# Performance work log

Hardware: AMD Instinct MI355X
Metric: run time of the kernel (lower is better)

## Reference

```python
import jax, jax.numpy as jnp
import numpy as np

NUM_HEADS = 16
SOFTPLUS_EPS = 1e-4


def rotate_half(x):
    x1, x2 = jnp.split(x, 2, axis=-1)
    return jnp.concatenate((-x2, x1), axis=-1)


def setup_inputs() -> dict:
    key = jax.random.key(0)
    B, S, H = 1, 2048, 2048
    D = H // NUM_HEADS  # 128
    ks = jax.random.split(key, 5)
    hidden_states = jax.random.normal(ks[0], (B, S, H), dtype=jnp.float32)
    # standard RoPE tables: [S, D]
    inv_freq = 1.0 / (10000.0 ** (np.arange(0, D, 2, dtype=np.float32) / D))
    freqs = np.outer(np.arange(S, dtype=np.float32), inv_freq)  # [S, D/2]
    emb = np.concatenate([freqs, freqs], axis=-1)  # [S, D]
    cos = jnp.asarray(np.cos(emb), dtype=jnp.float32)
    sin = jnp.asarray(np.sin(emb), dtype=jnp.float32)
    std = 0.02
    w_q = jax.random.normal(ks[1], (2 * H, H), dtype=jnp.float32) * std
    w_k = jax.random.normal(ks[2], (2 * H, H), dtype=jnp.float32) * std
    w_v = jax.random.normal(ks[3], (H, H), dtype=jnp.float32) * std
    w_o = jax.random.normal(ks[4], (H, H), dtype=jnp.float32) * std
    return {"hidden_states": hidden_states, "cos": cos, "sin": sin,
            "w_q": w_q, "w_k": w_k, "w_v": w_v, "w_o": w_o}


def reference(hidden_states, cos, sin, w_q, w_k, w_v, w_o):
    B, S, H = hidden_states.shape
    NH = NUM_HEADS
    D = H // NH
    # projections (torch Linear: y = x @ W.T)
    q = (hidden_states @ w_q.T).reshape(B, S, NH, 2 * D).swapaxes(1, 2)  # [B,NH,S,2D]
    k = (hidden_states @ w_k.T).reshape(B, S, NH, 2 * D).swapaxes(1, 2)
    v = (hidden_states @ w_v.T).reshape(B, S, NH, D).swapaxes(1, 2)      # [B,NH,S,D]
    q_mu, q_sigma_raw = jnp.split(q, 2, axis=-1)
    k_mu, k_sigma_raw = jnp.split(k, 2, axis=-1)
    q_sigma = jax.nn.softplus(q_sigma_raw) + SOFTPLUS_EPS
    k_sigma = jax.nn.softplus(k_sigma_raw) + SOFTPLUS_EPS
    q_w = q_mu / jnp.sqrt(q_sigma)
    k_w = k_mu / jnp.sqrt(k_sigma)
    # RoPE on variance-weighted means; cos/sin [S,D] broadcast over [B,NH,S,D]
    q_w = q_w * cos + rotate_half(q_w) * sin
    k_w = k_w * cos + rotate_half(k_w) * sin
    q_sq = jnp.sum(q_w * q_w, axis=-1, keepdims=True)          # [B,NH,S,1]
    k_sq = jnp.sum(k_w * k_w, axis=-1, keepdims=True)          # [B,NH,S,1]
    dot = jnp.einsum('bhqd,bhkd->bhqk', q_w, k_w)              # [B,NH,S,S]
    weighted_dist = q_sq + jnp.swapaxes(k_sq, -2, -1) - 2.0 * dot
    log_det_q = jnp.sum(jnp.log(q_sigma), axis=-1, keepdims=True)
    log_det_k = jnp.sum(jnp.log(k_sigma), axis=-1, keepdims=True)
    log_det = log_det_q + jnp.swapaxes(log_det_k, -2, -1)
    attn_scores = -0.5 * (weighted_dist + log_det)
    attn_probs = jax.nn.softmax(attn_scores, axis=-1)
    attn_out = jnp.einsum('bhqk,bhkd->bhqd', attn_probs, v)    # [B,NH,S,D]
    attn_out = attn_out.swapaxes(1, 2).reshape(B, S, H)
    return attn_out @ w_o.T
```

## Files before the change

### kernel.cpp

```cpp
#include <hip/hip_runtime.h>
#include <stdint.h>

#define S_LEN 2048
#define HID   2048
#define NHEAD 16
#define HD    128
#define NQK   8192
#define K_HID 2048

typedef _Float16 f16x8 __attribute__((ext_vector_type(8)));
typedef float    f32x4 __attribute__((ext_vector_type(4)));

__device__ __forceinline__ unsigned short f2h(float f) {
    _Float16 h = (_Float16)f;
    union { _Float16 h; unsigned short u; } c; c.h = h;
    return c.u;
}
__device__ __forceinline__ float h2f(unsigned short b) {
    union { unsigned short u; _Float16 h; } c; c.u = b;
    return (float)c.h;
}
__device__ __forceinline__ float softplus_f(float x) {
    return (x > 20.f) ? x : log1pf(expf(x));
}
__device__ __forceinline__ unsigned pk2h(float a, float b) {
    auto w = __builtin_amdgcn_cvt_pkrtz(a, b);
    union { decltype(w) h; unsigned u; } c; c.h = w;
    return c.u;
}
#define EXP2F(x) __builtin_amdgcn_exp2f(x)
#define LOG2E 1.44269504088896f
__device__ __forceinline__ void gload_lds16(const unsigned short* g, unsigned short* l) {
    __builtin_amdgcn_global_load_lds(
        (const __attribute__((address_space(1))) unsigned int*)g,
        (__attribute__((address_space(3))) unsigned int*)l, 16, 0, 0);
}
__device__ __forceinline__ void bar() {
    asm volatile("" ::: "memory");
    __builtin_amdgcn_s_barrier();
    asm volatile("" ::: "memory");
}
#define VMCNT(n) asm volatile("s_waitcnt vmcnt(" #n ")" ::: "memory")

__global__ __launch_bounds__(256) void cast5(const float* __restrict__ hs,
                                             const float* __restrict__ wq,
                                             const float* __restrict__ wk,
                                             const float* __restrict__ wv,
                                             const float* __restrict__ wo,
                                             unsigned short* __restrict__ hs16,
                                             unsigned short* __restrict__ wqk16,
                                             unsigned short* __restrict__ wv16,
                                             unsigned short* __restrict__ wo16) {
    int b = blockIdx.x;
    const float* src;
    unsigned short* dst;
    int i;
    if (b < 4096)       { src = hs; dst = hs16;                          i = b; }
    else if (b < 12288) { src = wq; dst = wqk16;                         i = b - 4096; }
    else if (b < 20480) { src = wk; dst = wqk16 + (size_t)4096 * K_HID;  i = b - 12288; }
    else if (b < 24576) { src = wv; dst = wv16;                          i = b - 20480; }
    else                { src = wo; dst = wo16;                          i = b - 24576; }
    int idx = i * 256 + threadIdx.x;
    float4 v = ((const float4*)src)[idx];
    ushort4 o;
    o.x = f2h(v.x); o.y = f2h(v.y); o.z = f2h(v.z); o.w = f2h(v.w);
    ((ushort4*)dst)[idx] = o;
}

template <bool OUT_F16>
__device__ __forceinline__ void gemm_body(const unsigned short* __restrict__ A,
                                          const unsigned short* __restrict__ B,
                                          void* __restrict__ Cv,
                                          int m0, int n0, int N,
                                          unsigned short* As, unsigned short* Bs) {
    const int t    = threadIdx.x;
    const int wave = t >> 6;
    const int lane = t & 63;
    const int wm   = wave >> 1, wn = wave & 1;
    const int lrow = lane & 15, quad = lane >> 4;
    const int srow = lane >> 2;
    const int scol = (lane & 3) * 8;

    f32x4 acc[4][4];
    for (int i = 0; i < 4; ++i)
        for (int j = 0; j < 4; ++j)
            acc[i][j] = (f32x4){0.f, 0.f, 0.f, 0.f};

    for (int k0 = 0; k0 < K_HID; k0 += 32) {
        for (int c = 0; c < 2; ++c) {
            int ch = wave * 2 + c;
            int row = ch * 16 + srow;
            gload_lds16(A + (size_t)(m0 + row) * K_HID + k0 + scol, &As[ch * 512]);
            gload_lds16(B + (size_t)(n0 + row) * K_HID + k0 + scol, &Bs[ch * 512]);
        }
        __syncthreads();

        f16x8 af[4], bfr[4];
        for (int tm = 0; tm < 4; ++tm)
            af[tm]  = *(const f16x8*)(&As[(wm * 64 + tm * 16 + lrow) * 32 + quad * 8]);
        for (int tn = 0; tn < 4; ++tn)
            bfr[tn] = *(const f16x8*)(&Bs[(wn * 64 + tn * 16 + lrow) * 32 + quad * 8]);
        for (int tm = 0; tm < 4; ++tm)
            for (int tn = 0; tn < 4; ++tn)
                acc[tm][tn] = __builtin_amdgcn_mfma_f32_16x16x32_f16(af[tm], bfr[tn], acc[tm][tn], 0, 0, 0);
        __syncthreads();
    }

    for (int tm = 0; tm < 4; ++tm)
        for (int tn = 0; tn < 4; ++tn) {
            int col = n0 + wn * 64 + tn * 16 + lrow;
            for (int r = 0; r < 4; ++r) {
                int row = m0 + wm * 64 + tm * 16 + quad * 4 + r;
                if (OUT_F16)
                    ((unsigned short*)Cv)[(size_t)row * N + col] = f2h(acc[tm][tn][r]);
                else
                    ((float*)Cv)[(size_t)row * N + col] = acc[tm][tn][r];
            }
        }
}

__device__ __forceinline__ void prep_body(int gid, int lane,
                                          const unsigned short* __restrict__ qk,
                                          const float* __restrict__ cosb,
                                          const float* __restrict__ sinb,
                                          unsigned short* __restrict__ Q16,
                                          unsigned short* __restrict__ K16,
                                          float* __restrict__ kbias) {
    int h = gid >> 11;
    int s = gid & 2047;
    int d1 = lane, d2 = lane + 64;
    const unsigned short* row = qk + (size_t)s * NQK;
    float c1 = cosb[s * HD + d1], c2 = cosb[s * HD + d2];
    float s1 = sinb[s * HD + d1], s2 = sinb[s * HD + d2];
    size_t ob = ((size_t)h * S_LEN + s) * HD;

    {
        int base = h * 256;
        float mu1 = h2f(row[base + d1]),       mu2 = h2f(row[base + d2]);
        float sg1 = softplus_f(h2f(row[base + 128 + d1])) + 1e-4f;
        float sg2 = softplus_f(h2f(row[base + 128 + d2])) + 1e-4f;
        float w1 = mu1 * rsqrtf(sg1), w2 = mu2 * rsqrtf(sg2);
        float o1 = w1 * c1 - w2 * s1;
        float o2 = w2 * c2 + w1 * s2;
        Q16[ob + d1] = f2h(o1 * LOG2E);
        Q16[ob + d2] = f2h(o2 * LOG2E);
    }
    {
        int base = 4096 + h * 256;
        float mu1 = h2f(row[base + d1]),       mu2 = h2f(row[base + d2]);
        float sg1 = softplus_f(h2f(row[base + 128 + d1])) + 1e-4f;
        float sg2 = softplus_f(h2f(row[base + 128 + d2])) + 1e-4f;
        float w1 = mu1 * rsqrtf(sg1), w2 = mu2 * rsqrtf(sg2);
        float o1 = w1 * c1 - w2 * s1;
        float o2 = w2 * c2 + w1 * s2;
        unsigned short k1 = f2h(o1), k2 = f2h(o2);
        K16[ob + d1] = k1; K16[ob + d2] = k2;
        float r1 = h2f(k1), r2 = h2f(k2);
        float part = r1 * r1 + r2 * r2 + logf(sg1) + logf(sg2);
        for (int off = 32; off > 0; off >>= 1) part += __shfl_down(part, off);
        if (lane == 0) kbias[(size_t)h * S_LEN + s] = -0.5f * LOG2E * part;
    }
}

__global__ __launch_bounds__(256) void gemm_qkv(const unsigned short* __restrict__ hs16,
                                                const unsigned short* __restrict__ wqk16,
                                                const unsigned short* __restrict__ wv16,
                                                unsigned short* __restrict__ qk16,
                                                unsigned short* __restrict__ Vt) {
    __shared__ __align__(16) unsigned short As[128 * 32];
    __shared__ __align__(16) unsigned short Bs[128 * 32];
    int b = blockIdx.x;
    if (b < 1024) {
        gemm_body<true>(hs16, wqk16, qk16, (b >> 6) * 128, (b & 63) * 128, NQK, As, Bs);
    } else {
        b -= 1024;
        gemm_body<true>(wv16, hs16, Vt, (b >> 4) * 128, (b & 15) * 128, S_LEN, As, Bs);
    }
}

template <bool OUT_F16>
__global__ __launch_bounds__(256) void gemm_nt_f16(const unsigned short* __restrict__ A,
                                                   const unsigned short* __restrict__ B,
                                                   void* __restrict__ Cv,
                                                   int M, int N, int Kd) {
    __shared__ __align__(16) unsigned short As[128 * 32];
    __shared__ __align__(16) unsigned short Bs[128 * 32];
    gemm_body<OUT_F16>(A, B, Cv, blockIdx.y * 128, blockIdx.x * 128, N, As, Bs);
}

__global__ __launch_bounds__(256) void vt_prep(const unsigned short* __restrict__ wv16,
                                               const unsigned short* __restrict__ hs16,
                                               unsigned short* __restrict__ Vt,
                                               const unsigned short* __restrict__ qk16,
                                               const float* __restrict__ cosb,
                                               const float* __restrict__ sinb,
                                               unsigned short* __restrict__ Q16,
                                               unsigned short* __restrict__ K16,
                                               float* __restrict__ kbias) {
    __shared__ __align__(16) unsigned short As[128 * 32];
    __shared__ __align__(16) unsigned short Bs[128 * 32];
    int b = blockIdx.x;
    if (b < 256) {
        gemm_body<true>(wv16, hs16, Vt, (b >> 4) * 128, (b & 15) * 128, S_LEN, As, Bs);
    } else {
        int gid = (b - 256) * 4 + (threadIdx.x >> 6);
        prep_body(gid, threadIdx.x & 63, qk16, cosb, sinb, Q16, K16, kbias);
    }
}

__global__ __launch_bounds__(256) void prep_qk(const unsigned short* __restrict__ qk,
                                               const float* __restrict__ cosb,
                                               const float* __restrict__ sinb,
                                               unsigned short* __restrict__ Q16,
                                               unsigned short* __restrict__ K16,
                                               float* __restrict__ kbias) {
    int gid = blockIdx.x * 4 + (threadIdx.x >> 6);
    prep_body(gid, threadIdx.x & 63, qk, cosb, sinb, Q16, K16, kbias);
}

__global__ __launch_bounds__(512, 2) void gemm256_qk(const unsigned short* __restrict__ A,
                                                     const unsigned short* __restrict__ B,
                                                     unsigned short* __restrict__ C) {
    extern __shared__ __align__(16) unsigned short lds[];
    const int t    = threadIdx.x;
    const int wave = t >> 6;
    const int lane = t & 63;
    const int wm   = wave >> 2, wn = wave & 3;
    const int lrow = lane & 15, quad = lane >> 4;

    const int x  = blockIdx.x & 7;
    const int sl = blockIdx.x >> 3;
    const int tm = ((x >> 2) << 2) + (sl >> 3);
    const int tn = ((x & 3) << 3) + (sl & 7);
    const int m0 = tm << 8, n0 = tn << 8;

    const int srow = lane >> 2;
    const int scol = ((lane & 3) * 8) ^ ((lane >> 5) << 4);
    const unsigned short* Ag = A + (size_t)(m0 + wave * 16 + srow) * K_HID + scol;
    const unsigned short* Bg = B + (size_t)(n0 + wave * 16 + srow) * K_HID + scol;

    const int swz = (lrow * 32 + quad * 8) ^ ((lrow >> 3) << 4);

    f32x4 acc[8][4];
    #pragma unroll
    for (int i = 0; i < 8; ++i)
        #pragma unroll
        for (int j = 0; j < 4; ++j) acc[i][j] = (f32x4){0.f, 0.f, 0.f, 0.f};

    {
        unsigned short* la = lds + wave * 1024;
        gload_lds16(Ag,               la);
        gload_lds16(Ag + 32,          la + 512);
        gload_lds16(Ag + 262144,      la + 8192);
        gload_lds16(Ag + 262144 + 32, la + 8704);
        unsigned short* lb = la + 16384;
        gload_lds16(Bg,               lb);
        gload_lds16(Bg + 32,          lb + 512);
        gload_lds16(Bg + 262144,      lb + 8192);
        gload_lds16(Bg + 262144 + 32, lb + 8704);
    }
    VMCNT(0);
    bar();

    f16x8 ah[4][2], b01[2][2];

    const int NT = K_HID / 64;
    #pragma unroll 1
    for (int t2 = 0; t2 < NT; ++t2) {
        const int buf = t2 & 1;
        const unsigned short* Lb = lds + buf * 32768;
        unsigned short*       Ln = lds + (buf ^ 1) * 32768 + wave * 1024;
        const int k1  = (t2 + 1) * 64;
        const bool pre = (t2 < NT - 1);

        f16x8 al[4][2], b23[2][2];

        if (pre) {
            gload_lds16(Ag + k1,               Ln);
            gload_lds16(Ag + k1 + 32,          Ln + 512);
            gload_lds16(Ag + 262144 + k1,      Ln + 8192);
            gload_lds16(Ag + 262144 + k1 + 32, Ln + 8704);
        }
        #pragma unroll
        for (int i = 0; i < 4; ++i) {
            al[i][0] = *(const f16x8*)(Lb + (wm * 8 + i) * 1024 + swz);
            al[i][1] = *(const f16x8*)(Lb + (wm * 8 + i) * 1024 + 512 + swz);
        }
        if (t2) {
            __builtin_amdgcn_s_setprio(1);
            #pragma unroll
            for (int i = 0; i < 4; ++i)
                #pragma unroll
                for (int j = 0; j < 2; ++j) {
                    acc[4 + i][j] = __builtin_amdgcn_mfma_f32_16x16x32_f16(ah[i][0], b01[j][0], acc[4 + i][j], 0, 0, 0);
                    acc[4 + i][j] = __builtin_amdgcn_mfma_f32_16x16x32_f16(ah[i][1], b01[j][1], acc[4 + i][j], 0, 0, 0);
                }
            __builtin_amdgcn_s_setprio(0);
        }
        #pragma unroll
        for (int j = 0; j < 2; ++j) {
            b01[j][0] = *(const f16x8*)(Lb + 16384 + (wn * 4 + j) * 1024 + swz);
            b01[j][1] = *(const f16x8*)(Lb + 16384 + (wn * 4 + j) * 1024 + 512 + swz);
        }
        bar();

        if (pre) {
            gload_lds16(Bg + k1,               Ln + 16384);
            gload_lds16(Bg + k1 + 32,          Ln + 16896);
            gload_lds16(Bg + 262144 + k1,      Ln + 24576);
            gload_lds16(Bg + 262144 + k1 + 32, Ln + 25088);
        }
        #pragma unroll
        for (int j = 0; j < 2; ++j) {
            b23[j][0] = *(const f16x8*)(Lb + 16384 + (wn * 4 + 2 + j) * 1024 + swz);
            b23[j][1] = *(const f16x8*)(Lb + 16384 + (wn * 4 + 2 + j) * 1024 + 512 + swz);
        }
        __builtin_amdgcn_s_setprio(1);
        #pragma unroll
        for (int i = 0; i < 4; ++i)
            #pragma unroll
            for (int j = 0; j < 2; ++j) {
                acc[i][j] = __builtin_amdgcn_mfma_f32_16x16x32_f16(al[i][0], b01[j][0], acc[i][j], 0, 0, 0);
                acc[i][j] = __builtin_amdgcn_mfma_f32_16x16x32_f16(al[i][1], b01[j][1], acc[i][j], 0, 0, 0);
            }
        __builtin_amdgcn_s_setprio(0);
        bar();

        #pragma unroll
        for (int i = 0; i < 4; ++i) {
            ah[i][0] = *(const f16x8*)(Lb + (wm * 8 + 4 + i) * 1024 + swz);
            ah[i][1] = *(const f16x8*)(Lb + (wm * 8 + 4 + i) * 1024 + 512 + swz);
        }
        __builtin_amdgcn_s_setprio(1);
        #pragma unroll
        for (int i = 0; i < 4; ++i)
            #pragma unroll
            for (int j = 0; j < 2; ++j) {
                acc[i][2 + j] = __builtin_amdgcn_mfma_f32_16x16x32_f16(al[i][0], b23[j][0], acc[i][2 + j], 0, 0, 0);
                acc[i][2 + j] = __builtin_amdgcn_mfma_f32_16x16x32_f16(al[i][1], b23[j][1], acc[i][2 + j], 0, 0, 0);
            }
        __builtin_amdgcn_s_setprio(0);
        bar();

        __builtin_amdgcn_s_setprio(1);
        #pragma unroll
        for (int i = 0; i < 4; ++i)
            #pragma unroll
            for (int j = 0; j < 2; ++j) {
                acc[4 + i][2 + j] = __builtin_amdgcn_mfma_f32_16x16x32_f16(ah[i][0], b23[j][0], acc[4 + i][2 + j], 0, 0, 0);
                acc[4 + i][2 + j] = __builtin_amdgcn_mfma_f32_16x16x32_f16(ah[i][1], b23[j][1], acc[4 + i][2 + j], 0, 0, 0);
            }
        __builtin_amdgcn_s_setprio(0);
        VMCNT(0);
        bar();
    }

    __builtin_amdgcn_s_setprio(1);
    #pragma unroll
    for (int i = 0; i < 4; ++i)
        #pragma unroll
        for (int j = 0; j < 2; ++j) {
            acc[4 + i][j] = __builtin_amdgcn_mfma_f32_16x16x32_f16(ah[i][0], b01[j][0], acc[4 + i][j], 0, 0, 0);
            acc[4 + i][j] = __builtin_amdgcn_mfma_f32_16x16x32_f16(ah[i][1], b01[j][1], acc[4 + i][j], 0, 0, 0);
        }
    __builtin_amdgcn_s_setprio(0);

    #pragma unroll
    for (int m = 0; m < 8; ++m)
        #pragma unroll
        for (int n = 0; n < 4; ++n) {
            const int col = n0 + wn * 64 + n * 16 + lrow;
            #pragma unroll
            for (int r = 0; r < 4; ++r) {
                const int row = m0 + wm * 128 + m * 16 + quad * 4 + r;
                C[(size_t)row * NQK + col] = f2h(acc[m][n][r]);
            }
        }
}

__global__ __launch_bounds__(256, 2) void flash_mfma(const unsigned short* __restrict__ Q16,
                                                     const unsigned short* __restrict__ K16,
                                                     const unsigned short* __restrict__ Vt,
                                                     const float* __restrict__ kbias,
                                                     unsigned short* __restrict__ OP,
                                                     float* __restrict__ ML) {
    constexpr int LV = 72;
    __shared__ __align__(16) unsigned short Khs[4 * 64 * 32];
    __shared__ __align__(16) unsigned short Vts[2 * 128 * 32];
    __shared__ __align__(16) unsigned short Ps[128 * LV];
    __shared__ float kb[64];

    const int t    = threadIdx.x;
    const int bb   = blockIdx.x;
    const int cc   = (bb & 7) | (((bb >> 7) & 3) << 3);
    const int h    = cc & 15;
    const int kz   = cc >> 4;
    const int q0   = ((bb >> 3) & 15) * 128;
    const int wave = t >> 6;
    const int lane = t & 63;
    const int lrow = lane & 15, quad = lane >> 4;
    const int srow = lane >> 2;
    const int scol = (lane & 3) * 8;

    f16x8 qf[2][4];
    for (int m = 0; m < 2; ++m) {
        size_t rb = ((size_t)h * S_LEN + q0 + wave * 32 + m * 16 + lrow) * HD;
        for (int kk = 0; kk < 4; ++kk)
            qf[m][kk] = *(const f16x8*)(Q16 + rb + kk * 32 + quad * 8);
    }

    float mrow[2], lsum[2];
    f32x4 Ofr[2][8];
    for (int m = 0; m < 2; ++m) { mrow[m] = -INFINITY; lsum[m] = 0.f; }
    for (int m = 0; m < 2; ++m)
        for (int d = 0; d < 8; ++d) Ofr[m][d] = (f32x4){0.f, 0.f, 0.f, 0.f};

    const int kbeg = kz * 1024;
    for (int k0 = kbeg; k0 < kbeg + 1024; k0 += 64) {
        {
            const unsigned short* kgb = K16 + ((size_t)h * S_LEN + k0) * HD;
            const unsigned short* vgb = Vt + ((size_t)h * HD) * S_LEN + k0;
            for (int c = 0; c < 4; ++c) {
                int ch = wave * 4 + c;
                int kk = ch >> 2;
                int r  = (ch & 3) * 16 + srow;
                gload_lds16(kgb + (size_t)r * HD + kk * 32 + scol, &Khs[ch * 512]);
                int kc = ch >> 3;
                int r2 = (ch & 7) * 16 + srow;
                gload_lds16(vgb + (size_t)r2 * S_LEN + kc * 32 + scol, &Vts[ch * 512]);
            }
            if (t < 64) kb[t] = kbias[(size_t)h * S_LEN + k0 + t];
        }
        __syncthreads();

        f32x4 kbv[4];
        #pragma unroll
        for (int nt = 0; nt < 4; ++nt)
            kbv[nt] = *(const f32x4*)(&kb[nt * 16 + quad * 4]);

        f32x4 sc[2][4];
        #pragma unroll
        for (int m = 0; m < 2; ++m)
            #pragma unroll
            for (int nt = 0; nt < 4; ++nt) sc[m][nt] = kbv[nt];
        for (int kk = 0; kk < 4; ++kk)
            for (int nt = 0; nt < 4; ++nt) {
                f16x8 khf = *(const f16x8*)(&Khs[kk * 2048 + (nt * 16 + lrow) * 32 + quad * 8]);
                sc[0][nt] = __builtin_amdgcn_mfma_f32_16x16x32_f16(khf, qf[0][kk], sc[0][nt], 0, 0, 0);
                sc[1][nt] = __builtin_amdgcn_mfma_f32_16x16x32_f16(khf, qf[1][kk], sc[1][nt], 0, 0, 0);
            }

        #pragma unroll
        for (int m = 0; m < 2; ++m) {
            float mx = -INFINITY;
            #pragma unroll
            for (int nt = 0; nt < 4; ++nt)
                #pragma unroll
                for (int r = 0; r < 4; ++r)
                    mx = fmaxf(mx, sc[m][nt][r]);
            mx = fmaxf(mx, __shfl_xor(mx, 16));
            mx = fmaxf(mx, __shfl_xor(mx, 32));
            if (!__all(mx <= mrow[m])) {
                float mnew  = fmaxf(mrow[m], mx);
                float alpha = EXP2F(mrow[m] - mnew);
                mrow[m] = mnew;
                lsum[m] *= alpha;
                float av0 = __shfl(alpha, quad * 4 + 0);
                float av1 = __shfl(alpha, quad * 4 + 1);
                float av2 = __shfl(alpha, quad * 4 + 2);
                float av3 = __shfl(alpha, quad * 4 + 3);
                #pragma unroll
                for (int dt = 0; dt < 8; ++dt) {
                    Ofr[m][dt][0] *= av0;
                    Ofr[m][dt][1] *= av1;
                    Ofr[m][dt][2] *= av2;
                    Ofr[m][dt][3] *= av3;
                }
            }
            float psum = 0.f;
            unsigned pw[8];
            #pragma unroll
            for (int nt = 0; nt < 4; ++nt) {
                float p0 = EXP2F(sc[m][nt][0] - mrow[m]);
                float p1 = EXP2F(sc[m][nt][1] - mrow[m]);
                float p2 = EXP2F(sc[m][nt][2] - mrow[m]);
                float p3 = EXP2F(sc[m][nt][3] - mrow[m]);
                psum += (p0 + p1) + (p2 + p3);
                pw[nt * 2]     = pk2h(p0, p1);
                pw[nt * 2 + 1] = pk2h(p2, p3);
            }
            lsum[m] += psum;
            int prow = (wave * 32 + m * 16 + lrow) * LV;
            #pragma unroll
            for (int nt = 0; nt < 4; ++nt) {
                uint2 wv; wv.x = pw[nt * 2]; wv.y = pw[nt * 2 + 1];
                *(uint2*)(&Ps[prow + nt * 16 + quad * 4]) = wv;
            }
        }

        for (int c = 0; c < 2; ++c) {
            f16x8 pa0 = *(const f16x8*)(&Ps[(wave * 32 + lrow) * LV + c * 32 + quad * 8]);
            f16x8 pa1 = *(const f16x8*)(&Ps[(wave * 32 + 16 + lrow) * LV + c * 32 + quad * 8]);
            for (int dt = 0; dt < 8; ++dt) {
                f16x8 vb = *(const f16x8*)(&Vts[c * 4096 + (dt * 16 + lrow) * 32 + quad * 8]);
                Ofr[0][dt] = __builtin_amdgcn_mfma_f32_16x16x32_f16(pa0, vb, Ofr[0][dt], 0, 0, 0);
                Ofr[1][dt] = __builtin_amdgcn_mfma_f32_16x16x32_f16(pa1, vb, Ofr[1][dt], 0, 0, 0);
            }
        }
        __syncthreads();
    }

    size_t obase = (size_t)(kz * NHEAD + h) * S_LEN;
    for (int m = 0; m < 2; ++m) {
        float rs = lsum[m];
        rs += __shfl_xor(rs, 16);
        rs += __shfl_xor(rs, 32);
        if (quad == 0) {
            int qrow = q0 + wave * 32 + m * 16 + lrow;
            ML[(obase + qrow) * 2]     = mrow[m];
            ML[(obase + qrow) * 2 + 1] = rs;
        }
        for (int r = 0; r < 4; ++r) {
            int qrow = q0 + wave * 32 + m * 16 + quad * 4 + r;
            unsigned short* op = OP + (obase + qrow) * HD;
            for (int dt = 0; dt < 8; ++dt)
                op[dt * 16 + lrow] = f2h(Ofr[m][dt][r]);
        }
    }
}

__global__ __launch_bounds__(256) void flash_merge(const unsigned short* __restrict__ OP,
                                                   const float* __restrict__ ML,
                                                   unsigned short* __restrict__ Obf) {
    int row = blockIdx.x * 2 + (threadIdx.x >> 7);
    int d   = threadIdx.x & 127;
    int h = row >> 11, q = row & 2047;
    size_t i0 = (size_t)h * S_LEN + q;
    size_t i1 = (size_t)(NHEAD + h) * S_LEN + q;
    float m0 = ML[i0 * 2], l0 = ML[i0 * 2 + 1];
    float m1 = ML[i1 * 2], l1 = ML[i1 * 2 + 1];
    float mf = fmaxf(m0, m1);
    float w0 = EXP2F(m0 - mf), w1 = EXP2F(m1 - mf);
    float inv = 1.f / (l0 * w0 + l1 * w1);
    float o = (h2f(OP[i0 * HD + d]) * w0 + h2f(OP[i1 * HD + d]) * w1) * inv;
    Obf[(size_t)q * HID + h * HD + d] = f2h(o);
}

extern "C" void kernel_launch(void* const* d_in, const int* in_sizes, int n_in,
                              void* d_out, int out_size, void* d_ws, size_t ws_size,
                              hipStream_t stream) {
    const float* hs   = (const float*)d_in[0];
    const float* cosb = (const float*)d_in[1];
    const float* sinb = (const float*)d_in[2];
    const float* wq   = (const float*)d_in[3];
    const float* wk   = (const float*)d_in[4];
    const float* wv   = (const float*)d_in[5];
    const float* wo   = (const float*)d_in[6];
    float* out = (float*)d_out;
    char*  ws  = (char*)d_ws;

    unsigned short* w_qk16 = (unsigned short*)(ws);
    unsigned short* Q16    = (unsigned short*)(ws);
    unsigned short* K16    = (unsigned short*)(ws + 8388608);
    float*          kbias  = (float*)(ws + 16777216);
    unsigned short* qk16   = (unsigned short*)(ws + 33554432);
    unsigned short* OP     = (unsigned short*)(ws + 33554432);
    float*          ML     = (float*)(ws + 50331648);
    unsigned short* hs16   = (unsigned short*)(ws + 67108864);
    unsigned short* Obf    = (unsigned short*)(ws + 67108864);
    unsigned short* w_v16  = (unsigned short*)(ws + 75497472);
    unsigned short* w_o16  = (unsigned short*)(ws + 83886080);
    unsigned short* Vt     = (unsigned short*)(ws + 92274688);

    static int use256 = -1;
    if (use256 < 0) {
        hipError_t e = hipFuncSetAttribute((const void*)gemm256_qk,
                                           hipFuncAttributeMaxDynamicSharedMemorySize,
                                           131072);
        use256 = (e == hipSuccess) ? 1 : 0;
    }

    cast5<<<28672, 256, 0, stream>>>(hs, wq, wk, wv, wo, hs16, w_qk16, w_v16, w_o16);

    if (use256) {
        gemm256_qk<<<256, 512, 131072, stream>>>(hs16, w_qk16, qk16);
        vt_prep<<<256 + 8192, 256, 0, stream>>>(w_v16, hs16, Vt, qk16,
                                                cosb, sinb, Q16, K16, kbias);
    } else {
        gemm_qkv<<<1280, 256, 0, stream>>>(hs16, w_qk16, w_v16, qk16, Vt);
        prep_qk<<<(NHEAD * S_LEN) / 4, 256, 0, stream>>>(qk16, cosb, sinb,
                                                         Q16, K16, kbias);
    }

    flash_mfma<<<512, 256, 0, stream>>>(Q16, K16, Vt, kbias, OP, ML);
    flash_merge<<<(NHEAD * S_LEN) / 2, 256, 0, stream>>>(OP, ML, Obf);
    gemm_nt_f16<false><<<dim3(16, 16), 256, 0, stream>>>(Obf, w_o16, out, S_LEN, HID, K_HID);
}
```

Before: 369.9 us.

## Fuse split-KV merge into flash kernel via last-block atomic counter

Removes the separate flash_merge launch. Each flash block increments a per-(head, query-tile) counter after writing its partial output. The second of the two KV-split blocks to finish then merges both partials into Obf. The counters are zeroed inside vt_prep. This saves a kernel launch and the re-read pass, at the cost of a threadfence, an atomic and some serialized merge work in the tail blocks.

```diff
diff --git a/kernel.cpp b/kernel.cpp
--- a/kernel.cpp
+++ b/kernel.cpp
@@ -196,13 +196,15 @@
                                                const float* __restrict__ sinb,
                                                unsigned short* __restrict__ Q16,
                                                unsigned short* __restrict__ K16,
-                                               float* __restrict__ kbias) {
+                                               float* __restrict__ kbias,
+                                               unsigned int* __restrict__ cnt) {
     __shared__ __align__(16) unsigned short As[128 * 32];
     __shared__ __align__(16) unsigned short Bs[128 * 32];
     int b = blockIdx.x;
     if (b < 256) {
         gemm_body<true>(wv16, hs16, Vt, (b >> 4) * 128, (b & 15) * 128, S_LEN, As, Bs);
     } else {
+        if (b == 256 && cnt) cnt[threadIdx.x] = 0;
         int gid = (b - 256) * 4 + (threadIdx.x >> 6);
         prep_body(gid, threadIdx.x & 63, qk16, cosb, sinb, Q16, K16, kbias);
     }
@@ -383,12 +385,15 @@
                                                      const unsigned short* __restrict__ Vt,
                                                      const float* __restrict__ kbias,
                                                      unsigned short* __restrict__ OP,
-                                                     float* __restrict__ ML) {
+                                                     float* __restrict__ ML,
+                                                     unsigned int* __restrict__ cnt,
+                                                     unsigned short* __restrict__ Obf) {
     constexpr int LV = 72;
     __shared__ __align__(16) unsigned short Khs[4 * 64 * 32];
     __shared__ __align__(16) unsigned short Vts[2 * 128 * 32];
     __shared__ __align__(16) unsigned short Ps[128 * LV];
     __shared__ float kb[64];
+    __shared__ unsigned oldv;
 
     const int t    = threadIdx.x;
     const int bb   = blockIdx.x;
@@ -527,6 +532,37 @@
                 op[dt * 16 + lrow] = f2h(Ofr[m][dt][r]);
         }
     }
+
+    if (cnt) {
+        __threadfence();
+        __syncthreads();
+        if (t == 0) oldv = atomicAdd(&cnt[h * 16 + (q0 >> 7)], 1u);
+        __syncthreads();
+        if (oldv == 1) {
+            __threadfence();
+            for (int it = t; it < 2048; it += 256) {
+                int row = it >> 4;
+                int ck  = it & 15;
+                int q   = q0 + row;
+                size_t i0 = (size_t)h * S_LEN + q;
+                size_t i1 = (size_t)(NHEAD + h) * S_LEN + q;
+                float m0 = ML[i0 * 2], l0 = ML[i0 * 2 + 1];
+                float m1 = ML[i1 * 2], l1 = ML[i1 * 2 + 1];
+                float mf = fmaxf(m0, m1);
+                float w0 = EXP2F(m0 - mf), w1 = EXP2F(m1 - mf);
+                float inv = 1.f / (l0 * w0 + l1 * w1);
+                f16x8 v0 = *(const f16x8*)(OP + i0 * HD + ck * 8);
+                f16x8 v1 = *(const f16x8*)(OP + i1 * HD + ck * 8);
+                f16x8 o;
+                #pragma unroll
+                for (int j = 0; j < 8; ++j) {
+                    float ov = ((float)v0[j] * w0 + (float)v1[j] * w1) * inv;
+                    o[j] = (_Float16)ov;
+                }
+                *(f16x8*)(Obf + (size_t)q * HID + h * HD + ck * 8) = o;
+            }
+        }
+    }
 }
 
 __global__ __launch_bounds__(256) void flash_merge(const unsigned short* __restrict__ OP,
@@ -563,6 +599,7 @@
     unsigned short* Q16    = (unsigned short*)(ws);
     unsigned short* K16    = (unsigned short*)(ws + 8388608);
     float*          kbias  = (float*)(ws + 16777216);
+    unsigned int*   cnt    = (unsigned int*)(ws + 20971520);
     unsigned short* qk16   = (unsigned short*)(ws + 33554432);
     unsigned short* OP     = (unsigned short*)(ws + 33554432);
     float*          ML     = (float*)(ws + 50331648);
@@ -585,14 +622,16 @@
     if (use256) {
         gemm256_qk<<<256, 512, 131072, stream>>>(hs16, w_qk16, qk16);
         vt_prep<<<256 + 8192, 256, 0, stream>>>(w_v16, hs16, Vt, qk16,
-                                                cosb, sinb, Q16, K16, kbias);
+                                                cosb, sinb, Q16, K16, kbias, cnt);
+        flash_mfma<<<512, 256, 0, stream>>>(Q16, K16, Vt, kbias, OP, ML, cnt, Obf);
+        gemm_nt_f16<false><<<dim3(16, 16), 256, 0, stream>>>(Obf, w_o16, out, S_LEN, HID, K_HID);
     } else {
         gemm_qkv<<<1280, 256, 0, stream>>>(hs16, w_qk16, w_v16, qk16, Vt);
         prep_qk<<<(NHEAD * S_LEN) / 4, 256, 0, stream>>>(qk16, cosb, sinb,
                                                          Q16, K16, kbias);
-    }
-
-    flash_mfma<<<512, 256, 0, stream>>>(Q16, K16, Vt, kbias, OP, ML);
-    flash_merge<<<(NHEAD * S_LEN) / 2, 256, 0, stream>>>(OP, ML, Obf);
-    gemm_nt_f16<false><<<dim3(16, 16), 256, 0, stream>>>(Obf, w_o16, out, S_LEN, HID, K_HID);
-}
+        flash_mfma<<<512, 256, 0, stream>>>(Q16, K16, Vt, kbias, OP, ML,
+                                            (unsigned int*)nullptr, (unsigned short*)nullptr);
+        flash_merge<<<(NHEAD * S_LEN) / 2, 256, 0, stream>>>(OP, ML, Obf);
+        gemm_nt_f16<false><<<dim3(16, 16), 256, 0, stream>>>(Obf, w_o16, out, S_LEN, HID, K_HID);
+    }
+}
```

Result: slower. 474.6 us (+28.3%).
